# Kernel tuning notes

Hardware: AMD Instinct MI355X
Metric: run time of the kernel (lower is better)

Reference implementation:

```python
import jax, jax.numpy as jnp
import numpy as np

N_NODES = 10000
N_EDGES = 200000
F = 128
NB = 20
LN_EPS = 1e-5

act = jax.nn.silu

def mlp2(x, W1, b1, W2, b2):
    # two-layer MLP: Linear -> silu -> Linear (weights stored [in, out])
    h = act(jnp.dot(x, W1) + b1)
    return jnp.dot(h, W2) + b2

def mlp2_nobias(x, W1, W2):
    return jnp.dot(act(jnp.dot(x, W1)), W2)

def layernorm(x, g, b):
    mu = jnp.mean(x, axis=-1, keepdims=True)
    var = jnp.mean(jnp.square(x - mu), axis=-1, keepdims=True)
    return (x - mu) * jax.lax.rsqrt(var + LN_EPS) * g + b

def setup_inputs() -> dict:
    key = jax.random.key(0)
    ks = jax.random.split(key, 32)
    s = 1.0 / np.sqrt(F)
    d = {
        "atom_node": jax.random.normal(ks[0], (N_NODES, F), jnp.float32),
        "force_node": jax.random.normal(ks[1], (N_NODES, 3, F), jnp.float32),
        "disp_node": jax.random.normal(ks[2], (N_NODES, 3, F), jnp.float32),
        "disp_edge": jax.random.normal(ks[3], (N_EDGES, 3), jnp.float32),
        "dist_edge": jax.random.uniform(ks[4], (N_EDGES, NB), jnp.float32),
        "edge_index": jax.random.randint(ks[5], (2, N_EDGES), 0, N_NODES, jnp.int32),
        # inv_message_nodepart
        "nmp_W1": jax.random.normal(ks[6], (F, F), jnp.float32) * s,
        "nmp_b1": jnp.zeros((F,), jnp.float32),
        "nmp_W2": jax.random.normal(ks[7], (F, F), jnp.float32) * s,
        "nmp_b2": jnp.zeros((F,), jnp.float32),
        # inv_message_edgepart
        "emp_W": jax.random.normal(ks[8], (NB, F), jnp.float32) * (1.0 / np.sqrt(NB)),
        "emp_b": jnp.zeros((F,), jnp.float32),
        # equiv_message1
        "eq1_W1": jax.random.normal(ks[9], (F, F), jnp.float32) * s,
        "eq1_b1": jnp.zeros((F,), jnp.float32),
        "eq1_W2": jax.random.normal(ks[10], (F, F), jnp.float32) * s,
        "eq1_b2": jnp.zeros((F,), jnp.float32),
        # equiv_message2
        "eq2_W1": jax.random.normal(ks[11], (F, F), jnp.float32) * s,
        "eq2_b1": jnp.zeros((F,), jnp.float32),
        "eq2_W2": jax.random.normal(ks[12], (F, F), jnp.float32) * s,
        "eq2_b2": jnp.zeros((F,), jnp.float32),
        # equiv_message3 (no bias)
        "eq3_W1": jax.random.normal(ks[13], (F, F), jnp.float32) * s,
        "eq3_W2": jax.random.normal(ks[14], (F, F), jnp.float32) * s,
        # inv_update
        "upd_W1": jax.random.normal(ks[15], (F, F), jnp.float32) * s,
        "upd_b1": jnp.zeros((F,), jnp.float32),
        "upd_W2": jax.random.normal(ks[16], (F, F), jnp.float32) * s,
        "upd_b2": jnp.zeros((F,), jnp.float32),
        # LayerNorm
        "ln_g": jnp.ones((F,), jnp.float32),
        "ln_b": jnp.zeros((F,), jnp.float32),
    }
    return d

def reference(atom_node, force_node, disp_node, disp_edge, dist_edge, edge_index,
              nmp_W1, nmp_b1, nmp_W2, nmp_b2, emp_W, emp_b,
              eq1_W1, eq1_b1, eq1_W2, eq1_b2,
              eq2_W1, eq2_b1, eq2_W2, eq2_b2,
              eq3_W1, eq3_W2,
              upd_W1, upd_b1, upd_W2, upd_b2,
              ln_g, ln_b):
    n = atom_node.shape[0]
    src = edge_index[0]
    dst = edge_index[1]
    seg = lambda x: jax.ops.segment_sum(x, src, num_segments=n)

    # invariant message: edge part * node parts gathered at both endpoints
    h = mlp2(atom_node, nmp_W1, nmp_b1, nmp_W2, nmp_b2)            # [N, F]
    e = jnp.dot(dist_edge, emp_W) + emp_b                           # [E, F]
    inv_message = e * h[src] * h[dst]                               # [E, F]
    atom_node = atom_node + seg(inv_message)

    # equivariant message 1: radial MLP * displacement vectors
    eq1 = mlp2(inv_message, eq1_W1, eq1_b1, eq1_W2, eq1_b2)[:, None, :] \
          * disp_edge[:, :, None]                                   # [E, 3, F]
    agg1 = seg(eq1)                                                 # [N, 3, F]
    force_node = force_node + agg1

    # equivariant message 2: edge MLP * neighbor displacement features (pre-update)
    eq2 = mlp2(inv_message, eq2_W1, eq2_b1, eq2_W2, eq2_b2)[:, None, :] \
          * disp_node[dst]                                          # [E, 3, F]
    disp_node = disp_node + seg(eq2)

    # equivariant message 3: scatter-then-gather of agg1 with invariant gate
    eq3_inv = mlp2_nobias(atom_node, eq3_W1, eq3_W2)                # [N, F]
    eq3 = eq3_inv[dst][:, None, :] * agg1[dst]                      # [E, 3, F]
    disp_node = disp_node + seg(eq3)

    # invariant update coupling force and displacement channels
    inv_update = mlp2(atom_node, upd_W1, upd_b1, upd_W2, upd_b2) \
                 * jnp.sum(-force_node * disp_node, axis=-2)        # [N, F]
    atom_node = layernorm(atom_node + inv_update, ln_g, ln_b)
    return (atom_node, force_node, disp_node)
```

## Files before the change

### kernel.cpp

```cpp
#include <hip/hip_runtime.h>
#include <hip/hip_bf16.h>

#define F 128
#define NB 20
#define KP 32
#define HSTRIDE 136
#define HROWS_STRIDE 140

typedef __attribute__((ext_vector_type(8))) short short8;
typedef __attribute__((ext_vector_type(4))) short short4v;
typedef __attribute__((ext_vector_type(4))) float floatx4;

__device__ __forceinline__ float silu_f(float x) {
    return x * __builtin_amdgcn_rcpf(1.0f + __expf(-x));
}
__device__ __forceinline__ float bfs2f(short s) {
    unsigned int u = ((unsigned int)(unsigned short)s) << 16;
    float f; __builtin_memcpy(&f, &u, 4); return f;
}
__device__ __forceinline__ float lo_bf(unsigned int u) { return bfs2f((short)(u & 0xFFFF)); }
__device__ __forceinline__ float hi_bf(unsigned int u) { return bfs2f((short)(u >> 16)); }
__device__ __forceinline__ unsigned int pack_bf2(float d, float v) {
    __hip_bfloat16 db = __float2bfloat16(d), vb = __float2bfloat16(v);
    return (unsigned int)*(unsigned short*)&db
         | ((unsigned int)*(unsigned short*)&vb << 16);
}

__device__ __forceinline__ void stage_issue(const __hip_bfloat16* W, int t,
                                            short8 wreg[4]) {
#pragma unroll
    for (int r = 0; r < 4; ++r)
        wreg[r] = *(const short8*)(W + (size_t)(r * 512 + t) * 8);
}
__device__ __forceinline__ void stage_write_frag(__hip_bfloat16* wbuf, int t,
                                                 const short8 wreg[4]) {
#pragma unroll
    for (int r = 0; r < 4; ++r) {
        const int c0 = r * 512 + t;
        const int n = c0 >> 4, p = c0 & 15;
        const int ks = p >> 2;
        const int frag = ((n >> 6) * 4 + ((n >> 4) & 3)) * 4 + ks;
        const int lam = (((p & 3) * 16) + (n & 15)) ^ (ks << 1);
        *(short8*)(wbuf + (size_t)frag * 512 + lam * 8) = wreg[r];
    }
}

__global__ __launch_bounds__(512, 4) void mlp_staged_kernel(
    const __hip_bfloat16* __restrict__ X,
    const __hip_bfloat16* __restrict__ W1, const float* __restrict__ b1,
    const __hip_bfloat16* __restrict__ W2, const float* __restrict__ b2,
    __hip_bfloat16* __restrict__ Y)
{
    __shared__ __hip_bfloat16 hid[128 * HSTRIDE];
    __shared__ __hip_bfloat16 wbuf[32 * 512];
    const int t = threadIdx.x;
    const int wave = t >> 6;
    const int rg   = wave >> 1;
    const int wf   = wave & 1;
    const int lane = t & 63;
    const int quad = lane >> 4;
    const int l16  = lane & 15;
    const int eloc0 = rg * 32;
    const int e0 = blockIdx.x * 128 + eloc0;
    const int fbase = wf * 64;

    short8 bxk[4][2];
#pragma unroll
    for (int ks = 0; ks < 4; ++ks)
#pragma unroll
        for (int et = 0; et < 2; ++et)
            bxk[ks][et] = *(const short8*)(X + (size_t)(e0 + et * 16 + l16) * F
                                           + ks * 32 + quad * 8);

    short8 wreg[4];
    floatx4 acc[4][2];

    stage_issue(W1, t, wreg);
    stage_write_frag(wbuf, t, wreg);
    __syncthreads();

    stage_issue(W2, t, wreg);
    __builtin_amdgcn_sched_barrier(0);
#pragma unroll
    for (int ft = 0; ft < 4; ++ft)
#pragma unroll
        for (int et = 0; et < 2; ++et)
            acc[ft][et] = (floatx4){0.f, 0.f, 0.f, 0.f};
#pragma unroll
    for (int ks = 0; ks < 4; ++ks) {
        short8 aw[4];
#pragma unroll
        for (int ft = 0; ft < 4; ++ft)
            aw[ft] = *(const short8*)(wbuf + ((wf * 4 + ft) * 4 + ks) * 512
                                      + ((lane ^ (ks << 1)) * 8));
#pragma unroll
        for (int ft = 0; ft < 4; ++ft)
#pragma unroll
            for (int et = 0; et < 2; ++et)
                acc[ft][et] = __builtin_amdgcn_mfma_f32_16x16x32_bf16(
                    aw[ft], bxk[ks][et], acc[ft][et], 0, 0, 0);
    }
#pragma unroll
    for (int ft = 0; ft < 4; ++ft) {
        const int feat = fbase + ft * 16 + quad * 4;
        const floatx4 bv = *(const floatx4*)(b1 + feat);
#pragma unroll
        for (int et = 0; et < 2; ++et) {
            const int el = eloc0 + et * 16 + l16;
            __align__(8) __hip_bfloat16 tmp[4];
#pragma unroll
            for (int r = 0; r < 4; ++r)
                tmp[r] = __float2bfloat16(silu_f(acc[ft][et][r] + bv[r]));
            *(short4v*)(hid + (size_t)el * HSTRIDE + feat) = *(const short4v*)tmp;
        }
    }
    __syncthreads();
    stage_write_frag(wbuf, t, wreg);
    __syncthreads();

#pragma unroll
    for (int ft = 0; ft < 4; ++ft)
#pragma unroll
        for (int et = 0; et < 2; ++et)
            acc[ft][et] = (floatx4){0.f, 0.f, 0.f, 0.f};
#pragma unroll
    for (int ks = 0; ks < 4; ++ks) {
        const int k0 = ks * 32 + quad * 8;
        short8 bh[2], aw[4];
#pragma unroll
        for (int et = 0; et < 2; ++et)
            bh[et] = *(const short8*)(hid + (size_t)(eloc0 + et * 16 + l16) * HSTRIDE + k0);
#pragma unroll
        for (int ft = 0; ft < 4; ++ft)
            aw[ft] = *(const short8*)(wbuf + ((wf * 4 + ft) * 4 + ks) * 512
                                      + ((lane ^ (ks << 1)) * 8));
#pragma unroll
        for (int ft = 0; ft < 4; ++ft)
#pragma unroll
            for (int et = 0; et < 2; ++et)
                acc[ft][et] = __builtin_amdgcn_mfma_f32_16x16x32_bf16(
                    aw[ft], bh[et], acc[ft][et], 0, 0, 0);
    }
#pragma unroll
    for (int ft = 0; ft < 4; ++ft) {
        const int feat = fbase + ft * 16 + quad * 4;
        const floatx4 bv = *(const floatx4*)(b2 + feat);
#pragma unroll
        for (int et = 0; et < 2; ++et) {
            const int e = e0 + et * 16 + l16;
            __align__(8) __hip_bfloat16 tmp[4];
#pragma unroll
            for (int r = 0; r < 4; ++r)
                tmp[r] = __float2bfloat16(acc[ft][et][r] + bv[r]);
            *(short4v*)(Y + (size_t)e * F + feat) = *(const short4v*)tmp;
        }
    }
}

__global__ __launch_bounds__(512, 4) void dual_mlp2_kernel(
    const __hip_bfloat16* Xe,
    const __hip_bfloat16* __restrict__ W1a_e, const float* __restrict__ b1a_e,
    const __hip_bfloat16* __restrict__ W2a_e, const float* __restrict__ b2a_e,
    const __hip_bfloat16* __restrict__ W1b_e, const float* __restrict__ b1b_e,
    const __hip_bfloat16* __restrict__ W2b_e, const float* __restrict__ b2b_e,
    __hip_bfloat16* __restrict__ Q1e, __hip_bfloat16* Q2e, int ntile_e,
    const __hip_bfloat16* __restrict__ Xn,
    const __hip_bfloat16* __restrict__ W1a_n,
    const __hip_bfloat16* __restrict__ W2a_n,
    const __hip_bfloat16* __restrict__ W1b_n, const float* __restrict__ b1b_n,
    const __hip_bfloat16* __restrict__ W2b_n, const float* __restrict__ b2b_n,
    __hip_bfloat16* __restrict__ Q1n, float* __restrict__ Q2n)
{
    __shared__ __hip_bfloat16 hid[128 * HSTRIDE];
    __shared__ __hip_bfloat16 wbuf[32 * 512];
    const bool nn = (int)blockIdx.x >= ntile_e;
    const int tile = nn ? ((int)blockIdx.x - ntile_e) : (int)blockIdx.x;
    const __hip_bfloat16* X   = nn ? Xn : Xe;
    const __hip_bfloat16* W1a = nn ? W1a_n : W1a_e;
    const __hip_bfloat16* W2a = nn ? W2a_n : W2a_e;
    const __hip_bfloat16* W1b = nn ? W1b_n : W1b_e;
    const __hip_bfloat16* W2b = nn ? W2b_n : W2b_e;
    const float* b1a = nn ? nullptr : b1a_e;
    const float* b2a = nn ? nullptr : b2a_e;
    const float* b1b = nn ? b1b_n : b1b_e;
    const float* b2b = nn ? b2b_n : b2b_e;

    const int t = threadIdx.x;
    const int wave = t >> 6;
    const int rg   = wave >> 1;
    const int wf   = wave & 1;
    const int lane = t & 63;
    const int quad = lane >> 4;
    const int l16  = lane & 15;
    const int eloc0 = rg * 32;
    const int e0 = tile * 128 + eloc0;
    const int fbase = wf * 64;

    short8 bxk[4][2];
#pragma unroll
    for (int ks = 0; ks < 4; ++ks)
#pragma unroll
        for (int et = 0; et < 2; ++et)
            bxk[ks][et] = *(const short8*)(X + (size_t)(e0 + et * 16 + l16) * F
                                           + ks * 32 + quad * 8);

    short8 wreg[4];
    floatx4 acc[4][2];

    stage_issue(W1a, t, wreg);
    stage_write_frag(wbuf, t, wreg);
    __syncthreads();

    stage_issue(W2a, t, wreg);
    __builtin_amdgcn_sched_barrier(0);
#pragma unroll
    for (int ft = 0; ft < 4; ++ft)
#pragma unroll
        for (int et = 0; et < 2; ++et)
            acc[ft][et] = (floatx4){0.f, 0.f, 0.f, 0.f};
#pragma unroll
    for (int ks = 0; ks < 4; ++ks) {
        short8 aw[4];
#pragma unroll
        for (int ft = 0; ft < 4; ++ft)
            aw[ft] = *(const short8*)(wbuf + ((wf * 4 + ft) * 4 + ks) * 512
                                      + ((lane ^ (ks << 1)) * 8));
#pragma unroll
        for (int ft = 0; ft < 4; ++ft)
#pragma unroll
            for (int et = 0; et < 2; ++et)
                acc[ft][et] = __builtin_amdgcn_mfma_f32_16x16x32_bf16(
                    aw[ft], bxk[ks][et], acc[ft][et], 0, 0, 0);
    }
#pragma unroll
    for (int ft = 0; ft < 4; ++ft) {
        const int feat = fbase + ft * 16 + quad * 4;
        floatx4 bv = (floatx4){0.f, 0.f, 0.f, 0.f};
        if (b1a) bv = *(const floatx4*)(b1a + feat);
#pragma unroll
        for (int et = 0; et < 2; ++et) {
            const int el = eloc0 + et * 16 + l16;
            __align__(8) __hip_bfloat16 tmp[4];
#pragma unroll
            for (int r = 0; r < 4; ++r)
                tmp[r] = __float2bfloat16(silu_f(acc[ft][et][r] + bv[r]));
            *(short4v*)(hid + (size_t)el * HSTRIDE + feat) = *(const short4v*)tmp;
        }
    }
    __syncthreads();
    stage_write_frag(wbuf, t, wreg);
    __syncthreads();

    stage_issue(W1b, t, wreg);
    __builtin_amdgcn_sched_barrier(0);
#pragma unroll
    for (int ft = 0; ft < 4; ++ft)
#pragma unroll
        for (int et = 0; et < 2; ++et)
            acc[ft][et] = (floatx4){0.f, 0.f, 0.f, 0.f};
#pragma unroll
    for (int ks = 0; ks < 4; ++ks) {
        const int k0 = ks * 32 + quad * 8;
        short8 bh[2], aw[4];
#pragma unroll
        for (int et = 0; et < 2; ++et)
            bh[et] = *(const short8*)(hid + (size_t)(eloc0 + et * 16 + l16) * HSTRIDE + k0);
#pragma unroll
        for (int ft = 0; ft < 4; ++ft)
            aw[ft] = *(const short8*)(wbuf + ((wf * 4 + ft) * 4 + ks) * 512
                                      + ((lane ^ (ks << 1)) * 8));
#pragma unroll
        for (int ft = 0; ft < 4; ++ft)
#pragma unroll
            for (int et = 0; et < 2; ++et)
                acc[ft][et] = __builtin_amdgcn_mfma_f32_16x16x32_bf16(
                    aw[ft], bh[et], acc[ft][et], 0, 0, 0);
    }
#pragma unroll
    for (int ft = 0; ft < 4; ++ft) {
        const int feat = fbase + ft * 16 + quad * 4;
        floatx4 bv = (floatx4){0.f, 0.f, 0.f, 0.f};
        if (b2a) bv = *(const floatx4*)(b2a + feat);
#pragma unroll
        for (int et = 0; et < 2; ++et) {
            const int e = e0 + et * 16 + l16;
            __align__(8) __hip_bfloat16 tmp[4];
#pragma unroll
            for (int r = 0; r < 4; ++r)
                tmp[r] = __float2bfloat16(acc[ft][et][r] + bv[r]);
            *(short4v*)((nn ? Q1n : Q1e) + (size_t)e * F + feat) = *(const short4v*)tmp;
        }
    }
    __syncthreads();
    stage_write_frag(wbuf, t, wreg);
    __syncthreads();

    stage_issue(W2b, t, wreg);
    __builtin_amdgcn_sched_barrier(0);
#pragma unroll
    for (int ft = 0; ft < 4; ++ft)
#pragma unroll
        for (int et = 0; et < 2; ++et)
            acc[ft][et] = (floatx4){0.f, 0.f, 0.f, 0.f};
#pragma unroll
    for (int ks = 0; ks < 4; ++ks) {
        short8 aw[4];
#pragma unroll
        for (int ft = 0; ft < 4; ++ft)
            aw[ft] = *(const short8*)(wbuf + ((wf * 4 + ft) * 4 + ks) * 512
                                      + ((lane ^ (ks << 1)) * 8));
#pragma unroll
        for (int ft = 0; ft < 4; ++ft)
#pragma unroll
            for (int et = 0; et < 2; ++et)
                acc[ft][et] = __builtin_amdgcn_mfma_f32_16x16x32_bf16(
                    aw[ft], bxk[ks][et], acc[ft][et], 0, 0, 0);
    }
#pragma unroll
    for (int ft = 0; ft < 4; ++ft) {
        const int feat = fbase + ft * 16 + quad * 4;
        floatx4 bv = (floatx4){0.f, 0.f, 0.f, 0.f};
        if (b1b) bv = *(const floatx4*)(b1b + feat);
#pragma unroll
        for (int et = 0; et < 2; ++et) {
            const int el = eloc0 + et * 16 + l16;
            __align__(8) __hip_bfloat16 tmp[4];
#pragma unroll
            for (int r = 0; r < 4; ++r)
                tmp[r] = __float2bfloat16(silu_f(acc[ft][et][r] + bv[r]));
            *(short4v*)(hid + (size_t)el * HSTRIDE + feat) = *(const short4v*)tmp;
        }
    }
    __syncthreads();
    stage_write_frag(wbuf, t, wreg);
    __syncthreads();

#pragma unroll
    for (int ft = 0; ft < 4; ++ft)
#pragma unroll
        for (int et = 0; et < 2; ++et)
            acc[ft][et] = (floatx4){0.f, 0.f, 0.f, 0.f};
#pragma unroll
    for (int ks = 0; ks < 4; ++ks) {
        const int k0 = ks * 32 + quad * 8;
        short8 bh[2], aw[4];
#pragma unroll
        for (int et = 0; et < 2; ++et)
            bh[et] = *(const short8*)(hid + (size_t)(eloc0 + et * 16 + l16) * HSTRIDE + k0);
#pragma unroll
        for (int ft = 0; ft < 4; ++ft)
            aw[ft] = *(const short8*)(wbuf + ((wf * 4 + ft) * 4 + ks) * 512
                                      + ((lane ^ (ks << 1)) * 8));
#pragma unroll
        for (int ft = 0; ft < 4; ++ft)
#pragma unroll
            for (int et = 0; et < 2; ++et)
                acc[ft][et] = __builtin_amdgcn_mfma_f32_16x16x32_bf16(
                    aw[ft], bh[et], acc[ft][et], 0, 0, 0);
    }
#pragma unroll
    for (int ft = 0; ft < 4; ++ft) {
        const int feat = fbase + ft * 16 + quad * 4;
        floatx4 bv = (floatx4){0.f, 0.f, 0.f, 0.f};
        if (b2b) bv = *(const floatx4*)(b2b + feat);
#pragma unroll
        for (int et = 0; et < 2; ++et) {
            const int e = e0 + et * 16 + l16;
            if (!nn) {
                __align__(8) __hip_bfloat16 tmp[4];
#pragma unroll
                for (int r = 0; r < 4; ++r)
                    tmp[r] = __float2bfloat16(acc[ft][et][r] + bv[r]);
                *(short4v*)(Q2e + (size_t)e * F + feat) = *(const short4v*)tmp;
            } else {
                floatx4 v;
#pragma unroll
                for (int r = 0; r < 4; ++r) v[r] = acc[ft][et][r] + bv[r];
                *(floatx4*)(Q2n + (size_t)e * F + feat) = v;
            }
        }
    }
}

__global__ __launch_bounds__(256) void edge_inv_mfma_kernel(
    const __hip_bfloat16* __restrict__ dist_p,
    const __hip_bfloat16* __restrict__ empWt,
    const float* __restrict__ emp_b, const __hip_bfloat16* __restrict__ h,
    const int* __restrict__ src_p, const int* __restrict__ dst_p,
    __hip_bfloat16* __restrict__ Xbf, int E)
{
    __shared__ __hip_bfloat16 hrows[256 * HROWS_STRIDE];
    __shared__ int ridx[256];
    const int t = threadIdx.x;
    const int wave = t >> 6;
    const int lane = t & 63;
    const int quad = lane >> 4;
    const int l16  = lane & 15;
    const int e0b = blockIdx.x * 128;
    const int e0 = e0b + wave * 32;

    {
        const int le = (t < 128) ? t : (t - 128);
        const int e = e0b + le;
        const int idx = (e < E) ? ((t < 128) ? src_p[e] : dst_p[e]) : 0;
        ridx[t] = idx;
    }
    __syncthreads();

#pragma unroll
    for (int i = 0; i < 16; ++i) {
        const int idx = i * 256 + t;
        const int r = idx >> 4, part = idx & 15;
        const short8 v = *(const short8*)(h + (size_t)ridx[r] * F + part * 8);
        const short4v lo = __builtin_shufflevector(v, v, 0, 1, 2, 3);
        const short4v hi = __builtin_shufflevector(v, v, 4, 5, 6, 7);
        *(short4v*)(hrows + (size_t)r * HROWS_STRIDE + part * 8)     = lo;
        *(short4v*)(hrows + (size_t)r * HROWS_STRIDE + part * 8 + 4) = hi;
    }

    short8 bx[2], aw[8];
#pragma unroll
    for (int et = 0; et < 2; ++et)
        bx[et] = *(const short8*)(dist_p + (size_t)(e0 + et * 16 + l16) * KP + quad * 8);
#pragma unroll
    for (int ft = 0; ft < 8; ++ft)
        aw[ft] = *(const short8*)(empWt + (size_t)(ft * 16 + l16) * KP + quad * 8);

    floatx4 acc[8][2];
#pragma unroll
    for (int ft = 0; ft < 8; ++ft)
#pragma unroll
        for (int et = 0; et < 2; ++et)
            acc[ft][et] = __builtin_amdgcn_mfma_f32_16x16x32_bf16(
                aw[ft], bx[et], (floatx4){0.f, 0.f, 0.f, 0.f}, 0, 0, 0);

    __syncthreads();

    int eidx[2];
#pragma unroll
    for (int et = 0; et < 2; ++et) eidx[et] = e0 + et * 16 + l16;

#pragma unroll
    for (int ft = 0; ft < 8; ++ft) {
        const int feat = ft * 16 + quad * 4;
        const floatx4 bv = *(const floatx4*)(emp_b + feat);
#pragma unroll
        for (int et = 0; et < 2; ++et) {
            const int le = wave * 32 + et * 16 + l16;
            const short4v hs = *(const short4v*)(hrows + (size_t)le * HROWS_STRIDE + feat);
            const short4v hd = *(const short4v*)(hrows + (size_t)(128 + le) * HROWS_STRIDE + feat);
            const bool v = eidx[et] < E;
            __align__(8) __hip_bfloat16 tmp[4];
#pragma unroll
            for (int r = 0; r < 4; ++r) {
                const float m = v ? (acc[ft][et][r] + bv[r]) * bfs2f(hs[r]) * bfs2f(hd[r])
                                  : 0.0f;
                tmp[r] = __float2bfloat16(m);
            }
            *(short4v*)(Xbf + (size_t)eidx[et] * F + feat) = *(const short4v*)tmp;
        }
    }
}

__global__ void prep_all_kernel(
    const float* __restrict__ W0, const float* __restrict__ W1,
    const float* __restrict__ W2, const float* __restrict__ W3,
    const float* __restrict__ W4, const float* __restrict__ W5,
    const float* __restrict__ W6, const float* __restrict__ W7,
    const float* __restrict__ W8, const float* __restrict__ W9,
    const float* __restrict__ emp_W, const float* __restrict__ atom_node,
    __hip_bfloat16* __restrict__ Wt, __hip_bfloat16* __restrict__ empWt,
    __hip_bfloat16* __restrict__ atom_bf, __hip_bfloat16* __restrict__ atom_new_bf,
    int* __restrict__ counts, int nF, int nPadTot, int N)
{
    const int WTOT = 10 * F * F;
    const int ETOT = F * KP;
    const int S2 = WTOT + ETOT;
    const int S3 = S2 + nPadTot;
    const int S4 = S3 + (nPadTot - nF);
    const int total = S4 + N;
    const int stride = gridDim.x * blockDim.x;
    for (int i = blockIdx.x * blockDim.x + threadIdx.x; i < total; i += stride) {
        if (i < WTOT) {
            const int w = i >> 14;
            const int idx = i & (F * F - 1);
            const int n = idx >> 7, k = idx & 127;
            const float* W = (w == 0) ? W0 : (w == 1) ? W1 : (w == 2) ? W2
                           : (w == 3) ? W3 : (w == 4) ? W4 : (w == 5) ? W5
                           : (w == 6) ? W6 : (w == 7) ? W7 : (w == 8) ? W8 : W9;
            Wt[i] = __float2bfloat16(W[k * F + n]);
        } else if (i < S2) {
            const int j = i - WTOT;
            const int n = j >> 5, k = j & (KP - 1);
            empWt[j] = __float2bfloat16(k < NB ? emp_W[k * F + n] : 0.0f);
        } else if (i < S3) {
            const int j = i - S2;
            atom_bf[j] = __float2bfloat16(j < nF ? atom_node[j] : 0.0f);
        } else if (i < S4) {
            atom_new_bf[(i - S3) + nF] = __float2bfloat16(0.0f);
        } else {
            counts[i - S4] = 0;
        }
    }
}


__global__ void csr_count_kernel(const int* __restrict__ src,
                                 int* __restrict__ counts, int E) {
    const int stride = gridDim.x * blockDim.x;
    for (int e = blockIdx.x * blockDim.x + threadIdx.x; e < E; e += stride)
        atomicAdd(&counts[src[e]], 1);
}

__global__ __launch_bounds__(1024) void csr_scan_kernel(
    const int* __restrict__ counts, int* __restrict__ offsets,
    int* __restrict__ cursor, int N)
{
    constexpr int T = 1024;
    const int t = threadIdx.x;
    const int per = (N + T - 1) / T;
    const int base = t * per;
    int lsum = 0;
    for (int i = 0; i < per; ++i) {
        int idx = base + i;
        if (idx < N) lsum += counts[idx];
    }
    __shared__ int s[T];
    s[t] = lsum;
    __syncthreads();
    for (int off = 1; off < T; off <<= 1) {
        int v = (t >= off) ? s[t - off] : 0;
        __syncthreads();
        s[t] += v;
        __syncthreads();
    }
    int run = s[t] - lsum;
    for (int i = 0; i < per; ++i) {
        int idx = base + i;
        if (idx < N) {
            offsets[idx] = run;
            cursor[idx] = run;
            run += counts[idx];
        }
    }
    if (t == T - 1) offsets[N] = run;
}

__global__ void csr_perm_kernel(const int* __restrict__ src,
                                const int* __restrict__ dst,
                                const float* __restrict__ disp_edge,
                                const float* __restrict__ dist_edge,
                                int* __restrict__ cursor,
                                int* __restrict__ src_p,
                                int* __restrict__ dst_p,
                                float* __restrict__ de_p,
                                __hip_bfloat16* __restrict__ dist_p, int E) {
    const int stride = gridDim.x * blockDim.x;
    for (int e = blockIdx.x * blockDim.x + threadIdx.x; e < E; e += stride) {
        const int s = src[e];
        const int pos = atomicAdd(&cursor[s], 1);
        src_p[pos] = s;
        dst_p[pos] = dst[e];
        de_p[3 * pos + 0] = disp_edge[3 * e + 0];
        de_p[3 * pos + 1] = disp_edge[3 * e + 1];
        de_p[3 * pos + 2] = disp_edge[3 * e + 2];
        __align__(16) __hip_bfloat16 tmp[KP];
#pragma unroll
        for (int k = 0; k < KP; ++k)
            tmp[k] = __float2bfloat16(k < NB ? dist_edge[(size_t)e * NB + k] : 0.0f);
#pragma unroll
        for (int q = 0; q < 4; ++q)
            *(short8*)(dist_p + (size_t)pos * KP + q * 8) = ((const short8*)tmp)[q];
    }
}


__global__ __launch_bounds__(256) void gather_inv_kernel(
    const __hip_bfloat16* __restrict__ inv_msg, const int* __restrict__ offsets,
    const float* __restrict__ atom,
    float* __restrict__ atom_new, __hip_bfloat16* __restrict__ atom_new_bf, int N)
{
    const int n = blockIdx.x * 4 + (threadIdx.x >> 6);
    if (n >= N) return;
    const int f0 = (threadIdx.x & 63) * 2;
    const int p0 = offsets[n], p1 = offsets[n + 1];
    float a0 = 0.0f, a1 = 0.0f;
    for (int p = p0; p < p1; ++p) {
        const unsigned int u = *(const unsigned int*)(inv_msg + (size_t)p * F + f0);
        a0 += lo_bf(u);
        a1 += hi_bf(u);
    }
    const float2 av = *(const float2*)(atom + (size_t)n * F + f0);
    const float v0 = av.x + a0, v1 = av.y + a1;
    *(float2*)(atom_new + (size_t)n * F + f0) = make_float2(v0, v1);
    __hip_bfloat16 b0 = __float2bfloat16(v0), b1 = __float2bfloat16(v1);
    *(ushort2*)(atom_new_bf + (size_t)n * F + f0) =
        make_ushort2(*(unsigned short*)&b0, *(unsigned short*)&b1);
}

__global__ __launch_bounds__(256) void gather_eq1_kernel(
    const __hip_bfloat16* __restrict__ eqm, const float* __restrict__ de_p,
    const int* __restrict__ offsets,
    const float* __restrict__ force, const float* __restrict__ disp_node,
    const __hip_bfloat16* __restrict__ eq3i_bf,
    float* __restrict__ out_force, ushort2* __restrict__ pk, int N)
{
    const int n = blockIdx.x * 4 + (threadIdx.x >> 6);
    if (n >= N) return;
    const int f0 = (threadIdx.x & 63) * 2;
    const int p0 = offsets[n], p1 = offsets[n + 1];
    float a00 = 0.f, a01 = 0.f, a10 = 0.f, a11 = 0.f, a20 = 0.f, a21 = 0.f;
    for (int p = p0; p < p1; ++p) {
        const unsigned int u = *(const unsigned int*)(eqm + (size_t)p * F + f0);
        const float m0 = lo_bf(u), m1 = hi_bf(u);
        const float d0 = de_p[(size_t)p * 3 + 0];
        const float d1 = de_p[(size_t)p * 3 + 1];
        const float d2 = de_p[(size_t)p * 3 + 2];
        a00 = fmaf(m0, d0, a00); a01 = fmaf(m1, d0, a01);
        a10 = fmaf(m0, d1, a10); a11 = fmaf(m1, d1, a11);
        a20 = fmaf(m0, d2, a20); a21 = fmaf(m1, d2, a21);
    }
    const unsigned int ug = *(const unsigned int*)(eq3i_bf + (size_t)n * F + f0);
    const float g0 = lo_bf(ug), g1 = hi_bf(ug);
    const size_t b = (size_t)n * 3 * F + f0;

    float2 f;
    f = *(const float2*)(force + b);
    *(float2*)(out_force + b) = make_float2(f.x + a00, f.y + a01);
    f = *(const float2*)(force + b + F);
    *(float2*)(out_force + b + F) = make_float2(f.x + a10, f.y + a11);
    f = *(const float2*)(force + b + 2 * F);
    *(float2*)(out_force + b + 2 * F) = make_float2(f.x + a20, f.y + a21);

    float2 dn;
    dn = *(const float2*)(disp_node + b);
    *(uint2*)(pk + b) = make_uint2(pack_bf2(dn.x, g0 * a00), pack_bf2(dn.y, g1 * a01));
    dn = *(const float2*)(disp_node + b + F);
    *(uint2*)(pk + b + F) = make_uint2(pack_bf2(dn.x, g0 * a10), pack_bf2(dn.y, g1 * a11));
    dn = *(const float2*)(disp_node + b + 2 * F);
    *(uint2*)(pk + b + 2 * F) = make_uint2(pack_bf2(dn.x, g0 * a20), pack_bf2(dn.y, g1 * a21));
}

__global__ __launch_bounds__(256) void gather_eq23_ln_kernel(
    const __hip_bfloat16* __restrict__ eqm2, const ushort2* __restrict__ pk,
    const float* __restrict__ disp_node,
    const int* __restrict__ dst_p, const int* __restrict__ offsets,
    const float* __restrict__ atom_new, const float* __restrict__ upd,
    const float* __restrict__ out_force,
    const float* __restrict__ ln_g, const float* __restrict__ ln_b,
    float* __restrict__ out_disp, float* __restrict__ out_atom, int N)
{
    const int n = blockIdx.x * 4 + (threadIdx.x >> 6);
    if (n >= N) return;
    const int f0 = (threadIdx.x & 63) * 2;
    const int p0 = offsets[n], p1 = offsets[n + 1];
    float a00 = 0.f, a01 = 0.f, a10 = 0.f, a11 = 0.f, a20 = 0.f, a21 = 0.f;
    int d = (p0 < p1) ? dst_p[p0] : 0;
    for (int p = p0; p < p1; ++p) {
        const int dn = (p + 1 < p1) ? dst_p[p + 1] : 0;
        const unsigned int u = *(const unsigned int*)(eqm2 + (size_t)p * F + f0);
        const float m0 = lo_bf(u), m1 = hi_bf(u);
        const size_t pb = (size_t)d * 3 * F + f0;
        const uint2 c0 = *(const uint2*)(pk + pb);
        const uint2 c1 = *(const uint2*)(pk + pb + F);
        const uint2 c2 = *(const uint2*)(pk + pb + 2 * F);
        a00 += m0 * lo_bf(c0.x) + hi_bf(c0.x);
        a01 += m1 * lo_bf(c0.y) + hi_bf(c0.y);
        a10 += m0 * lo_bf(c1.x) + hi_bf(c1.x);
        a11 += m1 * lo_bf(c1.y) + hi_bf(c1.y);
        a20 += m0 * lo_bf(c2.x) + hi_bf(c2.x);
        a21 += m1 * lo_bf(c2.y) + hi_bf(c2.y);
        d = dn;
    }
    const size_t b = (size_t)n * 3 * F + f0;
    float2 dn2;
    dn2 = *(const float2*)(disp_node + b);
    const float2 od0 = make_float2(dn2.x + a00, dn2.y + a01);
    dn2 = *(const float2*)(disp_node + b + F);
    const float2 od1 = make_float2(dn2.x + a10, dn2.y + a11);
    dn2 = *(const float2*)(disp_node + b + 2 * F);
    const float2 od2 = make_float2(dn2.x + a20, dn2.y + a21);
    *(float2*)(out_disp + b)         = od0;
    *(float2*)(out_disp + b + F)     = od1;
    *(float2*)(out_disp + b + 2 * F) = od2;

    const float2 fo0 = *(const float2*)(out_force + b);
    const float2 fo1 = *(const float2*)(out_force + b + F);
    const float2 fo2 = *(const float2*)(out_force + b + 2 * F);
    const float s0 = -(fo0.x * od0.x + fo1.x * od1.x + fo2.x * od2.x);
    const float s1 = -(fo0.y * od0.y + fo1.y * od1.y + fo2.y * od2.y);

    const float2 an = *(const float2*)(atom_new + (size_t)n * F + f0);
    const float2 up = *(const float2*)(upd + (size_t)n * F + f0);
    const float y0 = an.x + up.x * s0;
    const float y1 = an.y + up.y * s1;

    float sy = y0 + y1, syy = y0 * y0 + y1 * y1;
#pragma unroll
    for (int m = 1; m < 64; m <<= 1) {
        sy  += __shfl_xor(sy, m);
        syy += __shfl_xor(syy, m);
    }
    const float mu = sy * (1.0f / F);
    float var = syy * (1.0f / F) - mu * mu;
    if (var < 0.0f) var = 0.0f;
    const float rstd = rsqrtf(var + 1e-5f);

    const float2 gg = *(const float2*)(ln_g + f0);
    const float2 bb = *(const float2*)(ln_b + f0);
    *(float2*)(out_atom + (size_t)n * F + f0) =
        make_float2((y0 - mu) * rstd * gg.x + bb.x,
                    (y1 - mu) * rstd * gg.y + bb.y);
}

extern "C" void kernel_launch(void* const* d_in, const int* in_sizes, int n_in,
                              void* d_out, int out_size, void* d_ws, size_t ws_size,
                              hipStream_t stream)
{
    const float* atom_node  = (const float*)d_in[0];
    const float* force_node = (const float*)d_in[1];
    const float* disp_node  = (const float*)d_in[2];
    const float* disp_edge  = (const float*)d_in[3];
    const float* dist_edge  = (const float*)d_in[4];
    const int*   edge_index = (const int*)d_in[5];
    const float* nmp_W1 = (const float*)d_in[6];
    const float* nmp_b1 = (const float*)d_in[7];
    const float* nmp_W2 = (const float*)d_in[8];
    const float* nmp_b2 = (const float*)d_in[9];
    const float* emp_W  = (const float*)d_in[10];
    const float* emp_b  = (const float*)d_in[11];
    const float* eq1_W1 = (const float*)d_in[12];
    const float* eq1_b1 = (const float*)d_in[13];
    const float* eq1_W2 = (const float*)d_in[14];
    const float* eq1_b2 = (const float*)d_in[15];
    const float* eq2_W1 = (const float*)d_in[16];
    const float* eq2_b1 = (const float*)d_in[17];
    const float* eq2_W2 = (const float*)d_in[18];
    const float* eq2_b2 = (const float*)d_in[19];
    const float* eq3_W1 = (const float*)d_in[20];
    const float* eq3_W2 = (const float*)d_in[21];
    const float* upd_W1 = (const float*)d_in[22];
    const float* upd_b1 = (const float*)d_in[23];
    const float* upd_W2 = (const float*)d_in[24];
    const float* upd_b2 = (const float*)d_in[25];
    const float* ln_g   = (const float*)d_in[26];
    const float* ln_b   = (const float*)d_in[27];

    const int N = in_sizes[0] / F;
    const int E = in_sizes[4] / NB;
    const int Mp  = ((E + 127) / 128) * 128;
    const int Mp2 = ((N + 127) / 128) * 128;
    const int* src = edge_index;
    const int* dst = edge_index + E;
    const int nF = N * F, n3F = N * 3 * F;

    float* out_atom  = (float*)d_out;
    float* out_force = out_atom + (size_t)nF;
    float* out_disp  = out_force + (size_t)n3F;

    char* p = (char*)d_ws;
    int* counts  = (int*)p;
    int* offsets = counts + N;
    int* cursor  = offsets + (N + 1);
    int* src_p   = cursor + N;
    int* dst_p   = src_p + E;
    size_t off = (size_t)(3 * N + 1 + 2 * E) * sizeof(int);
    off = (off + 63) & ~(size_t)63;
    float* de_p = (float*)(p + off); off += (size_t)3 * E * sizeof(float);
    off = (off + 63) & ~(size_t)63;
    __hip_bfloat16* dist_p = (__hip_bfloat16*)(p + off); off += (size_t)Mp * KP * 2;
    __hip_bfloat16* empWt  = (__hip_bfloat16*)(p + off); off += (size_t)F * KP * 2;

    __hip_bfloat16* h_bf        = (__hip_bfloat16*)(p + off); off += (size_t)Mp2 * F * 2;
    __hip_bfloat16* atom_bf     = (__hip_bfloat16*)(p + off); off += (size_t)Mp2 * F * 2;
    __hip_bfloat16* atom_new_bf = (__hip_bfloat16*)(p + off); off += (size_t)Mp2 * F * 2;
    __hip_bfloat16* eq3i_bf     = (__hip_bfloat16*)(p + off); off += (size_t)Mp2 * F * 2;
    off = (off + 63) & ~(size_t)63;
    float* atom_new = (float*)(p + off); off += (size_t)nF * 4;
    float* upd_f    = (float*)(p + off); off += (size_t)Mp2 * F * 4;
    ushort2* pk     = (ushort2*)(p + off); off += (size_t)n3F * sizeof(ushort2);
    off = (off + 63) & ~(size_t)63;
    __hip_bfloat16* Xbf = (__hip_bfloat16*)(p + off); off += (size_t)Mp * F * 2;
    __hip_bfloat16* Q1  = (__hip_bfloat16*)(p + off); off += (size_t)Mp * F * 2;
    __hip_bfloat16* Q2  = Xbf;
    __hip_bfloat16* Wt  = (__hip_bfloat16*)(p + off);
    __hip_bfloat16* Wt_eq1a = Wt + 0 * F * F;
    __hip_bfloat16* Wt_eq1b = Wt + 1 * F * F;
    __hip_bfloat16* Wt_eq2a = Wt + 2 * F * F;
    __hip_bfloat16* Wt_eq2b = Wt + 3 * F * F;
    __hip_bfloat16* Wt_nmpa = Wt + 4 * F * F;
    __hip_bfloat16* Wt_nmpb = Wt + 5 * F * F;
    __hip_bfloat16* Wt_eq3a = Wt + 6 * F * F;
    __hip_bfloat16* Wt_eq3b = Wt + 7 * F * F;
    __hip_bfloat16* Wt_upda = Wt + 8 * F * F;
    __hip_bfloat16* Wt_updb = Wt + 9 * F * F;

    prep_all_kernel<<<1024, 256, 0, stream>>>(
        eq1_W1, eq1_W2, eq2_W1, eq2_W2, nmp_W1, nmp_W2, eq3_W1, eq3_W2,
        upd_W1, upd_W2, emp_W, atom_node,
        Wt, empWt, atom_bf, atom_new_bf, counts, nF, Mp2 * F, N);

    csr_count_kernel<<<256, 256, 0, stream>>>(src, counts, E);
    csr_scan_kernel<<<1, 1024, 0, stream>>>(counts, offsets, cursor, N);
    csr_perm_kernel<<<256, 256, 0, stream>>>(src, dst, disp_edge, dist_edge,
                                             cursor, src_p, dst_p, de_p, dist_p, E);

    mlp_staged_kernel<<<Mp2 / 128, 512, 0, stream>>>(
        atom_bf, Wt_nmpa, nmp_b1, Wt_nmpb, nmp_b2, h_bf);

    edge_inv_mfma_kernel<<<Mp / 128, 256, 0, stream>>>(
        dist_p, empWt, emp_b, h_bf, src_p, dst_p, Xbf, E);
    gather_inv_kernel<<<(N + 3) / 4, 256, 0, stream>>>(Xbf, offsets, atom_node,
                                                       atom_new, atom_new_bf, N);

    {
        const int ntileE = Mp / 128;
        const int ntileN = Mp2 / 128;
        dual_mlp2_kernel<<<ntileE + ntileN, 512, 0, stream>>>(
            Xbf, Wt_eq1a, eq1_b1, Wt_eq1b, eq1_b2,
            Wt_eq2a, eq2_b1, Wt_eq2b, eq2_b2, Q1, Q2, ntileE,
            atom_new_bf, Wt_eq3a, Wt_eq3b,
            Wt_upda, upd_b1, Wt_updb, upd_b2, eq3i_bf, upd_f);
    }

    gather_eq1_kernel<<<(N + 3) / 4, 256, 0, stream>>>(
        Q1, de_p, offsets, force_node, disp_node, eq3i_bf, out_force, pk, N);
    gather_eq23_ln_kernel<<<(N + 3) / 4, 256, 0, stream>>>(
        Q2, pk, disp_node, dst_p, offsets, atom_new, upd_f, out_force,
        ln_g, ln_b, out_disp, out_atom, N);
}
```

Baseline: 412.7 us.

## Keep MLP hidden activations in registers via lane shuffles, double-buffer weight LDS

The dual MLP kernel now gives each wave 16 rows across all 128 output features instead of 32 rows by 64 features. This lets the silu hidden activations stay in registers as packed bf16 and be redistributed with cross-lane shuffles instead of going through a shared-memory hidden buffer. Weight staging alternates between two LDS buffers, which removes one barrier per stage. The cost is more registers (8 accumulators, 8 weight fragments, packed hidden values) and many shuffle instructions. Weights read from LDS are also reused across half as many rows per wave.

```diff
diff --git a/kernel.cpp b/kernel.cpp
--- a/kernel.cpp
+++ b/kernel.cpp
@@ -39,10 +39,33 @@
         const int c0 = r * 512 + t;
         const int n = c0 >> 4, p = c0 & 15;
         const int ks = p >> 2;
-        const int frag = ((n >> 6) * 4 + ((n >> 4) & 3)) * 4 + ks;
+        const int frag = (n >> 4) * 4 + ks;
         const int lam = (((p & 3) * 16) + (n & 15)) ^ (ks << 1);
         *(short8*)(wbuf + (size_t)frag * 512 + lam * 8) = wreg[r];
     }
+}
+
+__device__ __forceinline__ short8 hshuffle(const uint2 h0, const uint2 h1,
+                                           int quad, int l16) {
+    const int srcA = (2 * (quad & 1)) * 16 + l16;
+    const int srcB = srcA + 16;
+    const bool hi = (quad >> 1) & 1;
+    const unsigned a0x = (unsigned)__shfl((int)h0.x, srcA);
+    const unsigned a0y = (unsigned)__shfl((int)h0.y, srcA);
+    const unsigned a1x = (unsigned)__shfl((int)h1.x, srcA);
+    const unsigned a1y = (unsigned)__shfl((int)h1.y, srcA);
+    const unsigned b0x = (unsigned)__shfl((int)h0.x, srcB);
+    const unsigned b0y = (unsigned)__shfl((int)h0.y, srcB);
+    const unsigned b1x = (unsigned)__shfl((int)h1.x, srcB);
+    const unsigned b1y = (unsigned)__shfl((int)h1.y, srcB);
+    uint4 u;
+    u.x = hi ? a1x : a0x;
+    u.y = hi ? a1y : a0y;
+    u.z = hi ? b1x : b0x;
+    u.w = hi ? b1y : b0y;
+    short8 out;
+    __builtin_memcpy(&out, &u, 16);
+    return out;
 }
 
 __global__ __launch_bounds__(512, 4) void mlp_staged_kernel(
@@ -91,7 +114,7 @@
         short8 aw[4];
 #pragma unroll
         for (int ft = 0; ft < 4; ++ft)
-            aw[ft] = *(const short8*)(wbuf + ((wf * 4 + ft) * 4 + ks) * 512
+            aw[ft] = *(const short8*)(wbuf + (((wf * 4 + ft) * 4) + ks) * 512
                                       + ((lane ^ (ks << 1)) * 8));
 #pragma unroll
         for (int ft = 0; ft < 4; ++ft)
@@ -132,7 +155,7 @@
             bh[et] = *(const short8*)(hid + (size_t)(eloc0 + et * 16 + l16) * HSTRIDE + k0);
 #pragma unroll
         for (int ft = 0; ft < 4; ++ft)
-            aw[ft] = *(const short8*)(wbuf + ((wf * 4 + ft) * 4 + ks) * 512
+            aw[ft] = *(const short8*)(wbuf + (((wf * 4 + ft) * 4) + ks) * 512
                                       + ((lane ^ (ks << 1)) * 8));
 #pragma unroll
         for (int ft = 0; ft < 4; ++ft)
@@ -157,7 +180,7 @@
     }
 }
 
-__global__ __launch_bounds__(512, 4) void dual_mlp2_kernel(
+__global__ __launch_bounds__(512, 4) void dual_mlp3_kernel(
     const __hip_bfloat16* Xe,
     const __hip_bfloat16* __restrict__ W1a_e, const float* __restrict__ b1a_e,
     const __hip_bfloat16* __restrict__ W2a_e, const float* __restrict__ b2a_e,
@@ -171,8 +194,8 @@
     const __hip_bfloat16* __restrict__ W2b_n, const float* __restrict__ b2b_n,
     __hip_bfloat16* __restrict__ Q1n, float* __restrict__ Q2n)
 {
-    __shared__ __hip_bfloat16 hid[128 * HSTRIDE];
-    __shared__ __hip_bfloat16 wbuf[32 * 512];
+    __shared__ __hip_bfloat16 wbuf0[32 * 512];
+    __shared__ __hip_bfloat16 wbuf1[32 * 512];
     const bool nn = (int)blockIdx.x >= ntile_e;
     const int tile = nn ? ((int)blockIdx.x - ntile_e) : (int)blockIdx.x;
     const __hip_bfloat16* X   = nn ? Xn : Xe;
@@ -187,197 +210,146 @@
 
     const int t = threadIdx.x;
     const int wave = t >> 6;
-    const int rg   = wave >> 1;
-    const int wf   = wave & 1;
     const int lane = t & 63;
     const int quad = lane >> 4;
     const int l16  = lane & 15;
-    const int eloc0 = rg * 32;
-    const int e0 = tile * 128 + eloc0;
-    const int fbase = wf * 64;
-
-    short8 bxk[4][2];
+    const int row  = tile * 128 + wave * 16 + l16;
+
+    short8 bxk[4];
 #pragma unroll
     for (int ks = 0; ks < 4; ++ks)
-#pragma unroll
-        for (int et = 0; et < 2; ++et)
-            bxk[ks][et] = *(const short8*)(X + (size_t)(e0 + et * 16 + l16) * F
-                                           + ks * 32 + quad * 8);
+        bxk[ks] = *(const short8*)(X + (size_t)row * F + ks * 32 + quad * 8);
 
     short8 wreg[4];
-    floatx4 acc[4][2];
+    floatx4 acc[8];
+    uint2 hpk[8];
 
     stage_issue(W1a, t, wreg);
-    stage_write_frag(wbuf, t, wreg);
+    stage_write_frag(wbuf0, t, wreg);
     __syncthreads();
 
     stage_issue(W2a, t, wreg);
     __builtin_amdgcn_sched_barrier(0);
 #pragma unroll
-    for (int ft = 0; ft < 4; ++ft)
-#pragma unroll
-        for (int et = 0; et < 2; ++et)
-            acc[ft][et] = (floatx4){0.f, 0.f, 0.f, 0.f};
+    for (int ft = 0; ft < 8; ++ft) acc[ft] = (floatx4){0.f, 0.f, 0.f, 0.f};
 #pragma unroll
     for (int ks = 0; ks < 4; ++ks) {
-        short8 aw[4];
-#pragma unroll
-        for (int ft = 0; ft < 4; ++ft)
-            aw[ft] = *(const short8*)(wbuf + ((wf * 4 + ft) * 4 + ks) * 512
+        short8 aw[8];
+#pragma unroll
+        for (int ft = 0; ft < 8; ++ft)
+            aw[ft] = *(const short8*)(wbuf0 + (ft * 4 + ks) * 512
                                       + ((lane ^ (ks << 1)) * 8));
 #pragma unroll
-        for (int ft = 0; ft < 4; ++ft)
-#pragma unroll
-            for (int et = 0; et < 2; ++et)
-                acc[ft][et] = __builtin_amdgcn_mfma_f32_16x16x32_bf16(
-                    aw[ft], bxk[ks][et], acc[ft][et], 0, 0, 0);
-    }
-#pragma unroll
-    for (int ft = 0; ft < 4; ++ft) {
-        const int feat = fbase + ft * 16 + quad * 4;
+        for (int ft = 0; ft < 8; ++ft)
+            acc[ft] = __builtin_amdgcn_mfma_f32_16x16x32_bf16(
+                aw[ft], bxk[ks], acc[ft], 0, 0, 0);
+    }
+#pragma unroll
+    for (int ft = 0; ft < 8; ++ft) {
+        const int feat = ft * 16 + quad * 4;
         floatx4 bv = (floatx4){0.f, 0.f, 0.f, 0.f};
         if (b1a) bv = *(const floatx4*)(b1a + feat);
-#pragma unroll
-        for (int et = 0; et < 2; ++et) {
-            const int el = eloc0 + et * 16 + l16;
-            __align__(8) __hip_bfloat16 tmp[4];
-#pragma unroll
-            for (int r = 0; r < 4; ++r)
-                tmp[r] = __float2bfloat16(silu_f(acc[ft][et][r] + bv[r]));
-            *(short4v*)(hid + (size_t)el * HSTRIDE + feat) = *(const short4v*)tmp;
-        }
-    }
-    __syncthreads();
-    stage_write_frag(wbuf, t, wreg);
+        const float v0 = silu_f(acc[ft][0] + bv[0]);
+        const float v1 = silu_f(acc[ft][1] + bv[1]);
+        const float v2 = silu_f(acc[ft][2] + bv[2]);
+        const float v3 = silu_f(acc[ft][3] + bv[3]);
+        hpk[ft] = make_uint2(pack_bf2(v0, v1), pack_bf2(v2, v3));
+    }
+    stage_write_frag(wbuf1, t, wreg);
     __syncthreads();
 
     stage_issue(W1b, t, wreg);
     __builtin_amdgcn_sched_barrier(0);
 #pragma unroll
-    for (int ft = 0; ft < 4; ++ft)
-#pragma unroll
-        for (int et = 0; et < 2; ++et)
-            acc[ft][et] = (floatx4){0.f, 0.f, 0.f, 0.f};
+    for (int ft = 0; ft < 8; ++ft) acc[ft] = (floatx4){0.f, 0.f, 0.f, 0.f};
 #pragma unroll
     for (int ks = 0; ks < 4; ++ks) {
-        const int k0 = ks * 32 + quad * 8;
-        short8 bh[2], aw[4];
-#pragma unroll
-        for (int et = 0; et < 2; ++et)
-            bh[et] = *(const short8*)(hid + (size_t)(eloc0 + et * 16 + l16) * HSTRIDE + k0);
-#pragma unroll
-        for (int ft = 0; ft < 4; ++ft)
-            aw[ft] = *(const short8*)(wbuf + ((wf * 4 + ft) * 4 + ks) * 512
+        const short8 bh = hshuffle(hpk[2 * ks], hpk[2 * ks + 1], quad, l16);
+        short8 aw[8];
+#pragma unroll
+        for (int ft = 0; ft < 8; ++ft)
+            aw[ft] = *(const short8*)(wbuf1 + (ft * 4 + ks) * 512
                                       + ((lane ^ (ks << 1)) * 8));
 #pragma unroll
-        for (int ft = 0; ft < 4; ++ft)
-#pragma unroll
-            for (int et = 0; et < 2; ++et)
-                acc[ft][et] = __builtin_amdgcn_mfma_f32_16x16x32_bf16(
-                    aw[ft], bh[et], acc[ft][et], 0, 0, 0);
-    }
-#pragma unroll
-    for (int ft = 0; ft < 4; ++ft) {
-        const int feat = fbase + ft * 16 + quad * 4;
+        for (int ft = 0; ft < 8; ++ft)
+            acc[ft] = __builtin_amdgcn_mfma_f32_16x16x32_bf16(
+                aw[ft], bh, acc[ft], 0, 0, 0);
+    }
+#pragma unroll
+    for (int ft = 0; ft < 8; ++ft) {
+        const int feat = ft * 16 + quad * 4;
         floatx4 bv = (floatx4){0.f, 0.f, 0.f, 0.f};
         if (b2a) bv = *(const floatx4*)(b2a + feat);
-#pragma unroll
-        for (int et = 0; et < 2; ++et) {
-            const int e = e0 + et * 16 + l16;
-            __align__(8) __hip_bfloat16 tmp[4];
-#pragma unroll
-            for (int r = 0; r < 4; ++r)
-                tmp[r] = __float2bfloat16(acc[ft][et][r] + bv[r]);
-            *(short4v*)((nn ? Q1n : Q1e) + (size_t)e * F + feat) = *(const short4v*)tmp;
-        }
-    }
-    __syncthreads();
-    stage_write_frag(wbuf, t, wreg);
+        __align__(8) __hip_bfloat16 tmp[4];
+#pragma unroll
+        for (int r = 0; r < 4; ++r)
+            tmp[r] = __float2bfloat16(acc[ft][r] + bv[r]);
+        *(short4v*)((nn ? Q1n : Q1e) + (size_t)row * F + feat) = *(const short4v*)tmp;
+    }
+    stage_write_frag(wbuf0, t, wreg);
     __syncthreads();
 
     stage_issue(W2b, t, wreg);
     __builtin_amdgcn_sched_barrier(0);
 #pragma unroll
-    for (int ft = 0; ft < 4; ++ft)
-#pragma unroll
-        for (int et = 0; et < 2; ++et)
-            acc[ft][et] = (floatx4){0.f, 0.f, 0.f, 0.f};
+    for (int ft = 0; ft < 8; ++ft) acc[ft] = (floatx4){0.f, 0.f, 0.f, 0.f};
 #pragma unroll
     for (int ks = 0; ks < 4; ++ks) {
-        short8 aw[4];
-#pragma unroll
-        for (int ft = 0; ft < 4; ++ft)
-            aw[ft] = *(const short8*)(wbuf + ((wf * 4 + ft) * 4 + ks) * 512
+        short8 aw[8];
+#pragma unroll
+        for (int ft = 0; ft < 8; ++ft)
+            aw[ft] = *(const short8*)(wbuf0 + (ft * 4 + ks) * 512
                                       + ((lane ^ (ks << 1)) * 8));
 #pragma unroll
-        for (int ft = 0; ft < 4; ++ft)
-#pragma unroll
-            for (int et = 0; et < 2; ++et)
-                acc[ft][et] = __builtin_amdgcn_mfma_f32_16x16x32_bf16(
-                    aw[ft], bxk[ks][et], acc[ft][et], 0, 0, 0);
-    }
-#pragma unroll
-    for (int ft = 0; ft < 4; ++ft) {
-        const int feat = fbase + ft * 16 + quad * 4;
+        for (int ft = 0; ft < 8; ++ft)
+            acc[ft] = __builtin_amdgcn_mfma_f32_16x16x32_bf16(
+                aw[ft], bxk[ks], acc[ft], 0, 0, 0);
+    }
+#pragma unroll
+    for (int ft = 0; ft < 8; ++ft) {
+        const int feat = ft * 16 + quad * 4;
         floatx4 bv = (floatx4){0.f, 0.f, 0.f, 0.f};
         if (b1b) bv = *(const floatx4*)(b1b + feat);
-#pragma unroll
-        for (int et = 0; et < 2; ++et) {
-            const int el = eloc0 + et * 16 + l16;
-            __align__(8) __hip_bfloat16 tmp[4];
-#pragma unroll
-            for (int r = 0; r < 4; ++r)
-                tmp[r] = __float2bfloat16(silu_f(acc[ft][et][r] + bv[r]));
-            *(short4v*)(hid + (size_t)el * HSTRIDE + feat) = *(const short4v*)tmp;
-        }
-    }
-    __syncthreads();
-    stage_write_frag(wbuf, t, wreg);
-    __syncthreads();
-
-#pragma unroll
-    for (int ft = 0; ft < 4; ++ft)
-#pragma unroll
-        for (int et = 0; et < 2; ++et)
-            acc[ft][et] = (floatx4){0.f, 0.f, 0.f, 0.f};
+        const float v0 = silu_f(acc[ft][0] + bv[0]);
+        const float v1 = silu_f(acc[ft][1] + bv[1]);
+        const float v2 = silu_f(acc[ft][2] + bv[2]);
+        const float v3 = silu_f(acc[ft][3] + bv[3]);
+        hpk[ft] = make_uint2(pack_bf2(v0, v1), pack_bf2(v2, v3));
+    }
+    stage_write_frag(wbuf1, t, wreg);
+    __syncthreads();
+
+#pragma unroll
+    for (int ft = 0; ft < 8; ++ft) acc[ft] = (floatx4){0.f, 0.f, 0.f, 0.f};
 #pragma unroll
     for (int ks = 0; ks < 4; ++ks) {
-        const int k0 = ks * 32 + quad * 8;
-        short8 bh[2], aw[4];
-#pragma unroll
-        for (int et = 0; et < 2; ++et)
-            bh[et] = *(const short8*)(hid + (size_t)(eloc0 + et * 16 + l16) * HSTRIDE + k0);
-#pragma unroll
-        for (int ft = 0; ft < 4; ++ft)
-            aw[ft] = *(const short8*)(wbuf + ((wf * 4 + ft) * 4 + ks) * 512
+        const short8 bh = hshuffle(hpk[2 * ks], hpk[2 * ks + 1], quad, l16);
+        short8 aw[8];
+#pragma unroll
+        for (int ft = 0; ft < 8; ++ft)
+            aw[ft] = *(const short8*)(wbuf1 + (ft * 4 + ks) * 512
                                       + ((lane ^ (ks << 1)) * 8));
 #pragma unroll
-        for (int ft = 0; ft < 4; ++ft)
-#pragma unroll
-            for (int et = 0; et < 2; ++et)
-                acc[ft][et] = __builtin_amdgcn_mfma_f32_16x16x32_bf16(
-                    aw[ft], bh[et], acc[ft][et], 0, 0, 0);
-    }
-#pragma unroll
-    for (int ft = 0; ft < 4; ++ft) {
-        const int feat = fbase + ft * 16 + quad * 4;
+        for (int ft = 0; ft < 8; ++ft)
+            acc[ft] = __builtin_amdgcn_mfma_f32_16x16x32_bf16(
+                aw[ft], bh, acc[ft], 0, 0, 0);
+    }
+#pragma unroll
+    for (int ft = 0; ft < 8; ++ft) {
+        const int feat = ft * 16 + quad * 4;
         floatx4 bv = (floatx4){0.f, 0.f, 0.f, 0.f};
         if (b2b) bv = *(const floatx4*)(b2b + feat);
-#pragma unroll
-        for (int et = 0; et < 2; ++et) {
-            const int e = e0 + et * 16 + l16;
-            if (!nn) {
-                __align__(8) __hip_bfloat16 tmp[4];
-#pragma unroll
-                for (int r = 0; r < 4; ++r)
-                    tmp[r] = __float2bfloat16(acc[ft][et][r] + bv[r]);
-                *(short4v*)(Q2e + (size_t)e * F + feat) = *(const short4v*)tmp;
-            } else {
-                floatx4 v;
-#pragma unroll
-                for (int r = 0; r < 4; ++r) v[r] = acc[ft][et][r] + bv[r];
-                *(floatx4*)(Q2n + (size_t)e * F + feat) = v;
-            }
+        if (!nn) {
+            __align__(8) __hip_bfloat16 tmp[4];
+#pragma unroll
+            for (int r = 0; r < 4; ++r)
+                tmp[r] = __float2bfloat16(acc[ft][r] + bv[r]);
+            *(short4v*)(Q2e + (size_t)row * F + feat) = *(const short4v*)tmp;
+        } else {
+            floatx4 v;
+#pragma unroll
+            for (int r = 0; r < 4; ++r) v[r] = acc[ft][r] + bv[r];
+            *(floatx4*)(Q2n + (size_t)row * F + feat) = v;
         }
     }
 }
@@ -816,7 +788,7 @@
     {
         const int ntileE = Mp / 128;
         const int ntileN = Mp2 / 128;
-        dual_mlp2_kernel<<<ntileE + ntileN, 512, 0, stream>>>(
+        dual_mlp3_kernel<<<ntileE + ntileN, 512, 0, stream>>>(
             Xbf, Wt_eq1a, eq1_b1, Wt_eq1b, eq1_b2,
             Wt_eq2a, eq2_b1, Wt_eq2b, eq2_b2, Q1, Q2, ntileE,
             atom_new_bf, Wt_eq3a, Wt_eq3b,
```

Measured after the change: 412.7 us (median of 2 runs). Within noise of the previous version (+0.0%).
